# Performance work log

Measured on AMD Instinct MI355X. Metric: run time of the kernel, lower is better.

The kernel has to match this reference:

```python
import jax, jax.numpy as jnp
import numpy as np

N = 50000   # nodes
E = 600000  # directed edges
B = 128     # graphs
IN = 128
H = 128
K = 30      # sort-pool k
C_OUT = 32
KER = 5
OUT_DIM = 10
L_OUT = K - KER + 1  # 26


def setup_inputs() -> dict:
    key = jax.random.key(0)
    ks = jax.random.split(key, 12)
    s = 0.05
    return {
        "x": jax.random.normal(ks[0], (N, IN), jnp.float32),
        "edge_index": jax.random.randint(ks[1], (2, E), 0, N),
        "batch": jnp.sort(jax.random.randint(ks[2], (N,), 0, B)),
        "W0": jax.random.normal(ks[3], (IN, H), jnp.float32) * s,
        "b0": jnp.zeros((H,), jnp.float32),
        "W1": jax.random.normal(ks[4], (H, H), jnp.float32) * s,
        "b1": jnp.zeros((H,), jnp.float32),
        "W2": jax.random.normal(ks[5], (H, H), jnp.float32) * s,
        "b2": jnp.zeros((H,), jnp.float32),
        "conv_w": jax.random.normal(ks[6], (C_OUT, H, KER), jnp.float32) * s,
        "conv_b": jnp.zeros((C_OUT,), jnp.float32),
        "lin1_w": jax.random.normal(ks[7], (C_OUT * L_OUT, H), jnp.float32) * s,
        "lin1_b": jnp.zeros((H,), jnp.float32),
        "lin2_w": jax.random.normal(ks[8], (H, OUT_DIM), jnp.float32) * s,
        "lin2_b": jnp.zeros((OUT_DIM,), jnp.float32),
    }


def reference(x, edge_index, batch, W0, b0, W1, b1, W2, b2,
              conv_w, conv_b, lin1_w, lin1_b, lin2_w, lin2_b):
    # --- GCN normalization (A + I, symmetric deg^-1/2) ---
    loops = jnp.arange(N)
    row = jnp.concatenate([edge_index[0], loops])  # source
    col = jnp.concatenate([edge_index[1], loops])  # target (aggregation side)
    deg = jax.ops.segment_sum(jnp.ones_like(col, dtype=x.dtype), col, num_segments=N)
    dinv = jax.lax.rsqrt(jnp.maximum(deg, 1.0))
    norm = dinv[row] * dinv[col]  # [E+N]

    def gcn(h, W, b):
        hw = h @ W                                            # [N,H]
        msg = hw[row] * norm[:, None]                         # gather [E+N,H]
        return jax.ops.segment_sum(msg, col, num_segments=N) + b

    h = jax.nn.relu(gcn(x, W0, b0))
    h = jax.nn.relu(gcn(h, W1, b1))
    h = jax.nn.relu(gcn(h, W2, b2))

    # --- SortAggregation: per-graph sort by last channel (desc), top-K, zero-pad ---
    last = h[:, -1]
    order = jnp.lexsort((-last, batch))  # primary: batch, secondary: last desc
    hs = h[order]
    bs = batch[order]
    counts = jax.ops.segment_sum(jnp.ones((N,), jnp.int32), batch, num_segments=B)
    starts = jnp.cumsum(counts) - counts  # exclusive prefix sum
    rank = jnp.arange(N) - starts[bs]     # within-graph rank after sort
    r = jnp.where(rank < K, rank, K)      # overflow bucket K is discarded
    pooled = jnp.zeros((B, K + 1, H), h.dtype).at[bs, r].add(hs)[:, :K]  # [B,K,H]

    # --- conv1d head (NCH layout, matches torch view/transpose) ---
    xc = jnp.transpose(pooled, (0, 2, 1))  # [B,H,K]
    y = jax.lax.conv_general_dilated(xc, conv_w, (1,), "VALID",
                                     dimension_numbers=("NCH", "OIH", "NCH"))
    y = jax.nn.relu(y + conv_b[None, :, None])  # [B,C_OUT,L_OUT]
    y = y.reshape(B, -1)
    y = jax.nn.relu(y @ lin1_w + lin1_b)
    return y @ lin2_w + lin2_b  # [B,OUT_DIM]
```

## Files before the change

### kernel.cpp

```cpp
#include <hip/hip_runtime.h>
#include <math.h>

#define Nn 50000
#define Ee 600000
#define Bg 128
#define Hd 128
#define Kt 30
#define CO 32
#define KW 5
#define LOUT 26
#define CAP 2048
#define SCB 196
#define CVO 8

typedef float v2f __attribute__((ext_vector_type(2)));
typedef short bf16x8 __attribute__((ext_vector_type(8)));
typedef float f32x4 __attribute__((ext_vector_type(4)));

__device__ __forceinline__ unsigned short bfr(float v) {
    unsigned u = __builtin_bit_cast(unsigned, v);
    unsigned r = (u + 0x7FFFu + ((u >> 16) & 1u)) >> 16;
    return (unsigned short)r;
}
__device__ __forceinline__ float bff(unsigned short h) {
    unsigned u = ((unsigned)h) << 16;
    return __builtin_bit_cast(float, u);
}

__global__ void init_kernel(int* __restrict__ deg_i, int* __restrict__ cnt,
                            int* __restrict__ bstart,
                            const float* __restrict__ conv_w, float* __restrict__ wT2) {
    int i = blockIdx.x * 256 + threadIdx.x;
    if (i < Nn) { deg_i[i] = 1; cnt[i] = 0; }
    if (i <= Bg) bstart[i] = Nn;
    if (i < CO * KW * Hd) {
        int ci = i & 127;
        int r = i >> 7;
        int o = r / KW, k = r - o * KW;
        wT2[i] = conv_w[((size_t)o * Hd + ci) * KW + k];
    }
}

__global__ void wprep_kernel(const float* __restrict__ W0, const float* __restrict__ W1,
                             const float* __restrict__ W2,
                             ushort* __restrict__ Bph, ushort* __restrict__ Bpm,
                             ushort* __restrict__ Bpl) {
    int t = blockIdx.x * 256 + threadIdx.x;
    if (t >= 3 * 2048) return;
    int l = t >> 11;
    int r = t & 2047;
    int kc = r >> 9;
    int n = (r >> 6) & 7;
    int lane = r & 63;
    int m = lane & 15, kq = lane >> 4;
    const float* W = (l == 0) ? W0 : (l == 1) ? W1 : W2;
    int col = n * 16 + m;
    size_t off = ((size_t)l * 2048 + (size_t)((kc * 8 + n) * 64 + lane)) * 8;
#pragma unroll
    for (int j = 0; j < 8; ++j) {
        float v = W[(size_t)(kc * 32 + kq * 8 + j) * Hd + col];
        unsigned short h = bfr(v);
        float r1 = v - bff(h);
        unsigned short mid = bfr(r1);
        Bph[off + j] = h;
        Bpm[off + j] = mid;
        Bpl[off + j] = bfr(r1 - bff(mid));
    }
}

__global__ void count_kernel(const int* __restrict__ ei, const int* __restrict__ batch,
                             int* __restrict__ deg_i, int* __restrict__ bstart) {
    int i = blockIdx.x * 256 + threadIdx.x;
    if (i < Ee) atomicAdd(&deg_i[ei[Ee + i]], 1);
    if (i < Nn) {
        int b = batch[i];
        if (i == 0) {
            bstart[b] = 0;
        } else {
            int bp = batch[i - 1];
            if (bp != b) bstart[b] = i;
        }
    }
}

__global__ __launch_bounds__(256) void scanA_kernel(const int* __restrict__ deg_i,
                            float* __restrict__ dinv, int* __restrict__ bsum) {
    __shared__ int s[256];
    int tid = threadIdx.x;
    int i = blockIdx.x * 256 + tid;
    int v = 0;
    if (i < Nn) {
        int d = deg_i[i];
        dinv[i] = 1.0f / sqrtf((float)d);
        v = d - 1;
    }
    s[tid] = v;
    __syncthreads();
    for (int off = 128; off > 0; off >>= 1) {
        if (tid < off) s[tid] += s[tid + off];
        __syncthreads();
    }
    if (tid == 0) bsum[blockIdx.x] = s[0];
}

__global__ __launch_bounds__(256) void scanB_kernel(const int* __restrict__ bsum,
                            int* __restrict__ boff, int* __restrict__ bstart) {
    __shared__ int s[256];
    int tid = threadIdx.x;
    int v = (tid < SCB) ? bsum[tid] : 0;
    s[tid] = v;
    __syncthreads();
    for (int off = 1; off < 256; off <<= 1) {
        int t = (tid >= off) ? s[tid - off] : 0;
        __syncthreads();
        s[tid] += t;
        __syncthreads();
    }
    if (tid < SCB) boff[tid] = s[tid] - v;
    if (tid == 0) {
        for (int b = Bg - 1; b >= 0; --b)
            if (bstart[b] == Nn) bstart[b] = bstart[b + 1];
    }
}

__global__ __launch_bounds__(256) void scanC_kernel(const int* __restrict__ deg_i,
                            const int* __restrict__ boff, int* __restrict__ row_ptr) {
    __shared__ int s[256];
    int tid = threadIdx.x;
    int i = blockIdx.x * 256 + tid;
    int v = (i < Nn) ? deg_i[i] - 1 : 0;
    s[tid] = v;
    __syncthreads();
    for (int off = 1; off < 256; off <<= 1) {
        int t = (tid >= off) ? s[tid - off] : 0;
        __syncthreads();
        s[tid] += t;
        __syncthreads();
    }
    if (i < Nn) row_ptr[i + 1] = s[tid] + boff[blockIdx.x];
    if (i == 0) row_ptr[0] = 0;
}

__global__ void fill_kernel(const int* __restrict__ ei, const int* __restrict__ row_ptr,
                            int* __restrict__ cnt, int* __restrict__ csr_src) {
    int e = blockIdx.x * 256 + threadIdx.x;
    if (e >= Ee) return;
    int c = ei[Ee + e];
    int r = ei[e];
    int p = row_ptr[c] + atomicAdd(&cnt[c], 1);
    csr_src[p] = r;
}

__global__ __launch_bounds__(256) void mmx_kernel(const float* __restrict__ Hin,
                            const ushort* __restrict__ Bph, const ushort* __restrict__ Bpm,
                            const ushort* __restrict__ Bpl,
                            const float* __restrict__ dinv, float* __restrict__ hw) {
    int tid = threadIdx.x;
    int w = tid >> 6, lane = tid & 63;
    int m = lane & 15, kq = lane >> 4;
    int rowA = blockIdx.x * 64 + w * 16 + m;
    bool va = rowA < Nn;
    const float* ap = Hin + (size_t)rowA * Hd;
    f32x4 acc[8];
#pragma unroll
    for (int n = 0; n < 8; ++n) acc[n] = (f32x4)0.f;
#pragma unroll
    for (int kc = 0; kc < 4; ++kc) {
        bf16x8 a0 = (bf16x8)0, a1 = (bf16x8)0, a2 = (bf16x8)0;
        if (va) {
            float av[8];
            *(float4*)&av[0] = *(const float4*)(ap + kc * 32 + kq * 8);
            *(float4*)&av[4] = *(const float4*)(ap + kc * 32 + kq * 8 + 4);
#pragma unroll
            for (int j = 0; j < 8; ++j) {
                unsigned short h = bfr(av[j]);
                float r1 = av[j] - bff(h);
                unsigned short mid = bfr(r1);
                a0[j] = (short)h;
                a1[j] = (short)mid;
                a2[j] = (short)bfr(r1 - bff(mid));
            }
        }
        const ushort* bhp = Bph + (size_t)((kc * 8) * 64 + lane) * 8;
        const ushort* bmp = Bpm + (size_t)((kc * 8) * 64 + lane) * 8;
        const ushort* blp = Bpl + (size_t)((kc * 8) * 64 + lane) * 8;
#pragma unroll
        for (int n = 0; n < 8; ++n) {
            bf16x8 b0 = *(const bf16x8*)(bhp + (size_t)n * 64 * 8);
            bf16x8 b1 = *(const bf16x8*)(bmp + (size_t)n * 64 * 8);
            bf16x8 b2 = *(const bf16x8*)(blp + (size_t)n * 64 * 8);
            acc[n] = __builtin_amdgcn_mfma_f32_16x16x32_bf16(a0, b0, acc[n], 0, 0, 0);
            acc[n] = __builtin_amdgcn_mfma_f32_16x16x32_bf16(a1, b0, acc[n], 0, 0, 0);
            acc[n] = __builtin_amdgcn_mfma_f32_16x16x32_bf16(a0, b1, acc[n], 0, 0, 0);
            acc[n] = __builtin_amdgcn_mfma_f32_16x16x32_bf16(a1, b1, acc[n], 0, 0, 0);
            acc[n] = __builtin_amdgcn_mfma_f32_16x16x32_bf16(a2, b0, acc[n], 0, 0, 0);
            acc[n] = __builtin_amdgcn_mfma_f32_16x16x32_bf16(a0, b2, acc[n], 0, 0, 0);
        }
    }
    int rbase = blockIdx.x * 64 + w * 16 + kq * 4;
#pragma unroll
    for (int reg = 0; reg < 4; ++reg) {
        int r = rbase + reg;
        if (r < Nn) {
            float s = dinv[r];
#pragma unroll
            for (int n = 0; n < 8; ++n)
                hw[(size_t)r * Hd + n * 16 + m] = acc[n][reg] * s;
        }
    }
}

__global__ __launch_bounds__(256) void agg_kernel(const float* __restrict__ hw,
                            const int* __restrict__ row_ptr, const int* __restrict__ csr_src,
                            const float* __restrict__ dinv, const float* __restrict__ bias,
                            float* __restrict__ hout) {
    int node = blockIdx.x * 4 + (threadIdx.x >> 6);
    if (node >= Nn) return;
    int lane = threadIdx.x & 63;
    const v2f* hw2 = (const v2f*)hw;
    v2f a0 = hw2[(size_t)node * 64 + lane];
    v2f a1 = 0.f, a2 = 0.f, a3 = 0.f;
    int e0 = row_ptr[node], e1 = row_ptr[node + 1];
    int e = e0;
    for (; e + 3 < e1; e += 4) {
        int s0 = __builtin_nontemporal_load(csr_src + e);
        int s1 = __builtin_nontemporal_load(csr_src + e + 1);
        int s2 = __builtin_nontemporal_load(csr_src + e + 2);
        int s3 = __builtin_nontemporal_load(csr_src + e + 3);
        a0 += hw2[(size_t)s0 * 64 + lane];
        a1 += hw2[(size_t)s1 * 64 + lane];
        a2 += hw2[(size_t)s2 * 64 + lane];
        a3 += hw2[(size_t)s3 * 64 + lane];
    }
    for (; e < e1; ++e) {
        int s0 = __builtin_nontemporal_load(csr_src + e);
        a0 += hw2[(size_t)s0 * 64 + lane];
    }
    v2f acc = (a0 + a1) + (a2 + a3);
    float d = dinv[node];
    v2f bv = ((const v2f*)bias)[lane];
    v2f o;
    o.x = fmaxf(fmaf(d, acc.x, bv.x), 0.f);
    o.y = fmaxf(fmaf(d, acc.y, bv.y), 0.f);
    ((v2f*)hout)[(size_t)node * 64 + lane] = o;
}

__global__ __launch_bounds__(256) void topk_kernel(const float* __restrict__ h,
                            const int* __restrict__ bstart, float* __restrict__ xcg) {
    __shared__ float vals[CAP];
    __shared__ float rv[4];
    __shared__ int ri[4];
    __shared__ int selS[Kt];
    int b = blockIdx.x, tid = threadIdx.x;
    int s0 = bstart[b], s1 = bstart[b + 1];
    int n = s1 - s0;
    int nc = n < CAP ? n : CAP;
    for (int j = tid; j < nc; j += 256)
        vals[j] = h[(size_t)(s0 + j) * Hd + (Hd - 1)];
    __syncthreads();
    for (int k = 0; k < Kt; ++k) {
        float bv = -1.f;
        int bi = 0x7fffffff;
        for (int j = tid; j < nc; j += 256) {
            float v = vals[j];
            if (v > bv || (v == bv && j < bi)) { bv = v; bi = j; }
        }
        for (int off = 32; off > 0; off >>= 1) {
            float ov = __shfl_down(bv, off);
            int oi = __shfl_down(bi, off);
            if (ov > bv || (ov == bv && oi < bi)) { bv = ov; bi = oi; }
        }
        int wid = tid >> 6;
        if ((tid & 63) == 0) { rv[wid] = bv; ri[wid] = bi; }
        __syncthreads();
        if (tid == 0) {
            float fv = rv[0]; int fi = ri[0];
            for (int w = 1; w < 4; ++w) {
                if (rv[w] > fv || (rv[w] == fv && ri[w] < fi)) { fv = rv[w]; fi = ri[w]; }
            }
            if (k < n) {
                selS[k] = s0 + fi;
                vals[fi] = -1.f;
            } else {
                selS[k] = -1;
            }
        }
        __syncthreads();
    }
    for (int i = tid; i < Kt * Hd; i += 256) {
        int t = i >> 7, c = i & 127;
        int s = selS[t];
        xcg[((size_t)b * Kt + t) * Hd + c] = (s >= 0) ? h[(size_t)s * Hd + c] : 0.f;
    }
}

__global__ __launch_bounds__(256) void conv_kernel(const float* __restrict__ xcg,
                            const float* __restrict__ wT2, const float* __restrict__ conv_b,
                            float* __restrict__ flatg) {
    __shared__ float xcl[Kt][130];
    int b = blockIdx.x, q = blockIdx.y;
    int o0 = q * CVO;
    int tid = threadIdx.x;
    for (int i = tid; i < Kt * 32; i += 256) {
        int t = i >> 5, c4 = i & 31;
        float4 v = ((const float4*)(xcg + ((size_t)b * Kt + t) * Hd))[c4];
        float2* dst = (float2*)&xcl[t][c4 * 4];
        dst[0] = make_float2(v.x, v.y);
        dst[1] = make_float2(v.z, v.w);
    }
    __syncthreads();
    int idx = tid;
    if (idx < CVO * LOUT) {
        int op = idx / LOUT, t = idx - op * LOUT;
        int o = o0 + op;
        float acc = conv_b[o];
#pragma unroll
        for (int k = 0; k < KW; ++k) {
            const float* xr = &xcl[t + k][0];
            const float* wr = wT2 + ((size_t)o * KW + k) * Hd;
#pragma unroll 8
            for (int c4 = 0; c4 < 32; ++c4) {
                float2 xa = *(const float2*)(xr + c4 * 4);
                float2 xb = *(const float2*)(xr + c4 * 4 + 2);
                float4 wv = *(const float4*)(wr + c4 * 4);
                acc = fmaf(xa.x, wv.x, acc);
                acc = fmaf(xa.y, wv.y, acc);
                acc = fmaf(xb.x, wv.z, acc);
                acc = fmaf(xb.y, wv.w, acc);
            }
        }
        flatg[((size_t)b * CO + o) * LOUT + t] = fmaxf(acc, 0.f);
    }
}

__global__ __launch_bounds__(256) void head2_kernel(const float* __restrict__ flatg,
                            const float* __restrict__ l1w, const float* __restrict__ l1b,
                            const float* __restrict__ l2w, const float* __restrict__ l2b,
                            float* __restrict__ out) {
    __shared__ float fl[CO * LOUT];
    __shared__ float pz[2][Hd];
    __shared__ float z[Hd];
    int b = blockIdx.x, tid = threadIdx.x;
    for (int i = tid; i < CO * LOUT; i += 256)
        fl[i] = flatg[(size_t)b * (CO * LOUT) + i];
    __syncthreads();
    int hh = tid & 127, half = tid >> 7;
    int m0 = half * 416;
    float acc = 0.f;
#pragma unroll 8
    for (int m = 0; m < 416; ++m)
        acc = fmaf(fl[m0 + m], l1w[(size_t)(m0 + m) * Hd + hh], acc);
    pz[half][hh] = acc;
    __syncthreads();
    if (tid < Hd)
        z[tid] = fmaxf(pz[0][tid] + pz[1][tid] + l1b[tid], 0.f);
    __syncthreads();
    if (tid < 10) {
        float a2 = l2b[tid];
        for (int j = 0; j < Hd; ++j)
            a2 = fmaf(z[j], l2w[j * 10 + tid], a2);
        out[b * 10 + tid] = a2;
    }
}

extern "C" void kernel_launch(void* const* d_in, const int* in_sizes, int n_in,
                              void* d_out, int out_size, void* d_ws, size_t ws_size,
                              hipStream_t stream) {
    const float* x      = (const float*)d_in[0];
    const int*   ei     = (const int*)d_in[1];
    const int*   batch  = (const int*)d_in[2];
    const float* W0     = (const float*)d_in[3];
    const float* b0     = (const float*)d_in[4];
    const float* W1     = (const float*)d_in[5];
    const float* b1     = (const float*)d_in[6];
    const float* W2     = (const float*)d_in[7];
    const float* b2     = (const float*)d_in[8];
    const float* conv_w = (const float*)d_in[9];
    const float* conv_b = (const float*)d_in[10];
    const float* l1w    = (const float*)d_in[11];
    const float* l1b    = (const float*)d_in[12];
    const float* l2w    = (const float*)d_in[13];
    const float* l2b    = (const float*)d_in[14];
    float* out = (float*)d_out;

    int* wsI = (int*)d_ws;
    size_t off = 0;
    int*   deg_i   = wsI + off; off += Nn;
    int*   cnt     = wsI + off; off += Nn;
    int*   row_ptr = wsI + off; off += 50004;
    int*   bstart  = wsI + off; off += 132;
    float* dinv    = (float*)(wsI + off); off += Nn;
    int*   bsum    = wsI + off; off += 256;
    int*   boff    = wsI + off; off += 256;
    int*   csr_src = wsI + off; off += Ee;
    off = (off + 3) & ~(size_t)3;
    ushort* Bph  = (ushort*)(wsI + off); off += 3 * 16384 / 2;
    ushort* Bpm  = (ushort*)(wsI + off); off += 3 * 16384 / 2;
    ushort* Bpl  = (ushort*)(wsI + off); off += 3 * 16384 / 2;
    float* hw    = (float*)(wsI + off); off += (size_t)Nn * Hd;
    float* hbuf  = (float*)(wsI + off); off += (size_t)Nn * Hd;
    float* xcg   = (float*)(wsI + off); off += (size_t)Bg * Kt * Hd;
    float* wT2   = (float*)(wsI + off); off += CO * KW * Hd;
    float* flatg = (float*)(wsI + off); off += (size_t)Bg * CO * LOUT;

    init_kernel<<<(Nn + 255) / 256, 256, 0, stream>>>(deg_i, cnt, bstart, conv_w, wT2);
    wprep_kernel<<<24, 256, 0, stream>>>(W0, W1, W2, Bph, Bpm, Bpl);
    count_kernel<<<(Ee + 255) / 256, 256, 0, stream>>>(ei, batch, deg_i, bstart);
    scanA_kernel<<<SCB, 256, 0, stream>>>(deg_i, dinv, bsum);
    scanB_kernel<<<1, 256, 0, stream>>>(bsum, boff, bstart);
    scanC_kernel<<<SCB, 256, 0, stream>>>(deg_i, boff, row_ptr);
    fill_kernel<<<(Ee + 255) / 256, 256, 0, stream>>>(ei, row_ptr, cnt, csr_src);

    dim3 mmGrid((Nn + 63) / 64);
    dim3 aggGrid((Nn + 3) / 4);
    mmx_kernel<<<mmGrid, 256, 0, stream>>>(x, Bph, Bpm, Bpl, dinv, hw);
    agg_kernel<<<aggGrid, 256, 0, stream>>>(hw, row_ptr, csr_src, dinv, b0, hbuf);
    mmx_kernel<<<mmGrid, 256, 0, stream>>>(hbuf, Bph + 16384, Bpm + 16384, Bpl + 16384, dinv, hw);
    agg_kernel<<<aggGrid, 256, 0, stream>>>(hw, row_ptr, csr_src, dinv, b1, hbuf);
    mmx_kernel<<<mmGrid, 256, 0, stream>>>(hbuf, Bph + 32768, Bpm + 32768, Bpl + 32768, dinv, hw);
    agg_kernel<<<aggGrid, 256, 0, stream>>>(hw, row_ptr, csr_src, dinv, b2, hbuf);

    topk_kernel<<<Bg, 256, 0, stream>>>(hbuf, bstart, xcg);
    conv_kernel<<<dim3(Bg, CO / CVO), 256, 0, stream>>>(xcg, wT2, conv_b, flatg);
    head2_kernel<<<Bg, 256, 0, stream>>>(flatg, l1w, l1b, l2w, l2b, out);
}
```

Measured before the change: 483.9 us.

## Fuse CSR build into cooperative kernel and merge tail kernels

Replaces the count/scan/fill sequence of five launches with one cooperative kernel that uses grid-wide syncs. The init and weight-prep kernels are merged into one launch. The top-k, conv and MLP head kernels become a single per-graph kernel that keeps intermediates in shared memory instead of global scratch. This cuts launch overhead and global round-trips, but the cooperative launch needs 1024 blocks resident at once, the conv stage now runs on only 128 blocks, and grid.sync adds its own cost.

```diff
diff --git a/kernel.cpp b/kernel.cpp
--- a/kernel.cpp
+++ b/kernel.cpp
@@ -1,5 +1,8 @@
 #include <hip/hip_runtime.h>
+#include <hip/hip_cooperative_groups.h>
 #include <math.h>
+
+namespace cg = cooperative_groups;
 
 #define Nn 50000
 #define Ee 600000
@@ -10,8 +13,7 @@
 #define KW 5
 #define LOUT 26
 #define CAP 2048
-#define SCB 196
-#define CVO 8
+#define CG_B 1024
 
 typedef float v2f __attribute__((ext_vector_type(2)));
 typedef short bf16x8 __attribute__((ext_vector_type(8)));
@@ -27,9 +29,13 @@
     return __builtin_bit_cast(float, u);
 }
 
-__global__ void init_kernel(int* __restrict__ deg_i, int* __restrict__ cnt,
+__global__ void initwprep_kernel(int* __restrict__ deg_i, int* __restrict__ cnt,
                             int* __restrict__ bstart,
-                            const float* __restrict__ conv_w, float* __restrict__ wT2) {
+                            const float* __restrict__ conv_w, float* __restrict__ wT2,
+                            const float* __restrict__ W0, const float* __restrict__ W1,
+                            const float* __restrict__ W2,
+                            ushort* __restrict__ Bph, ushort* __restrict__ Bpm,
+                            ushort* __restrict__ Bpl) {
     int i = blockIdx.x * 256 + threadIdx.x;
     if (i < Nn) { deg_i[i] = 1; cnt[i] = 0; }
     if (i <= Bg) bstart[i] = Nn;
@@ -39,116 +45,110 @@
         int o = r / KW, k = r - o * KW;
         wT2[i] = conv_w[((size_t)o * Hd + ci) * KW + k];
     }
-}
-
-__global__ void wprep_kernel(const float* __restrict__ W0, const float* __restrict__ W1,
-                             const float* __restrict__ W2,
-                             ushort* __restrict__ Bph, ushort* __restrict__ Bpm,
-                             ushort* __restrict__ Bpl) {
-    int t = blockIdx.x * 256 + threadIdx.x;
-    if (t >= 3 * 2048) return;
-    int l = t >> 11;
-    int r = t & 2047;
-    int kc = r >> 9;
-    int n = (r >> 6) & 7;
-    int lane = r & 63;
-    int m = lane & 15, kq = lane >> 4;
-    const float* W = (l == 0) ? W0 : (l == 1) ? W1 : W2;
-    int col = n * 16 + m;
-    size_t off = ((size_t)l * 2048 + (size_t)((kc * 8 + n) * 64 + lane)) * 8;
-#pragma unroll
-    for (int j = 0; j < 8; ++j) {
-        float v = W[(size_t)(kc * 32 + kq * 8 + j) * Hd + col];
-        unsigned short h = bfr(v);
-        float r1 = v - bff(h);
-        unsigned short mid = bfr(r1);
-        Bph[off + j] = h;
-        Bpm[off + j] = mid;
-        Bpl[off + j] = bfr(r1 - bff(mid));
-    }
-}
-
-__global__ void count_kernel(const int* __restrict__ ei, const int* __restrict__ batch,
-                             int* __restrict__ deg_i, int* __restrict__ bstart) {
-    int i = blockIdx.x * 256 + threadIdx.x;
-    if (i < Ee) atomicAdd(&deg_i[ei[Ee + i]], 1);
-    if (i < Nn) {
+    if (i < 3 * 2048) {
+        int l = i >> 11;
+        int r = i & 2047;
+        int kc = r >> 9;
+        int n = (r >> 6) & 7;
+        int lane = r & 63;
+        int m = lane & 15, kq = lane >> 4;
+        const float* W = (l == 0) ? W0 : (l == 1) ? W1 : W2;
+        int col = n * 16 + m;
+        size_t off = ((size_t)l * 2048 + (size_t)((kc * 8 + n) * 64 + lane)) * 8;
+#pragma unroll
+        for (int j = 0; j < 8; ++j) {
+            float v = W[(size_t)(kc * 32 + kq * 8 + j) * Hd + col];
+            unsigned short h = bfr(v);
+            float r1 = v - bff(h);
+            unsigned short mid = bfr(r1);
+            Bph[off + j] = h;
+            Bpm[off + j] = mid;
+            Bpl[off + j] = bfr(r1 - bff(mid));
+        }
+    }
+}
+
+__global__ __launch_bounds__(256, 4) void csr_coop(
+        const int* __restrict__ ei, const int* __restrict__ batch,
+        int* __restrict__ deg_i, int* __restrict__ bstart,
+        float* __restrict__ dinv, int* __restrict__ bsum, int* __restrict__ boff,
+        int* __restrict__ row_ptr, int* __restrict__ cnt, int* __restrict__ csr_src) {
+    cg::grid_group grid = cg::this_grid();
+    int tid = threadIdx.x;
+    int gtid = blockIdx.x * 256 + tid;
+    const int T = CG_B * 256;
+    __shared__ int ls[256];
+
+    for (int i = gtid; i < Ee; i += T)
+        atomicAdd(&deg_i[ei[Ee + i]], 1);
+    for (int i = gtid; i < Nn; i += T) {
         int b = batch[i];
-        if (i == 0) {
-            bstart[b] = 0;
-        } else {
-            int bp = batch[i - 1];
-            if (bp != b) bstart[b] = i;
-        }
-    }
-}
-
-__global__ __launch_bounds__(256) void scanA_kernel(const int* __restrict__ deg_i,
-                            float* __restrict__ dinv, int* __restrict__ bsum) {
-    __shared__ int s[256];
-    int tid = threadIdx.x;
-    int i = blockIdx.x * 256 + tid;
-    int v = 0;
-    if (i < Nn) {
-        int d = deg_i[i];
-        dinv[i] = 1.0f / sqrtf((float)d);
-        v = d - 1;
-    }
-    s[tid] = v;
-    __syncthreads();
-    for (int off = 128; off > 0; off >>= 1) {
-        if (tid < off) s[tid] += s[tid + off];
+        if (i == 0) bstart[b] = 0;
+        else if (batch[i - 1] != b) bstart[b] = i;
+    }
+    grid.sync();
+
+    {
+        int v = 0;
+        if (gtid < Nn) {
+            int d = deg_i[gtid];
+            dinv[gtid] = 1.0f / sqrtf((float)d);
+            v = d - 1;
+        }
+        ls[tid] = v;
         __syncthreads();
-    }
-    if (tid == 0) bsum[blockIdx.x] = s[0];
-}
-
-__global__ __launch_bounds__(256) void scanB_kernel(const int* __restrict__ bsum,
-                            int* __restrict__ boff, int* __restrict__ bstart) {
-    __shared__ int s[256];
-    int tid = threadIdx.x;
-    int v = (tid < SCB) ? bsum[tid] : 0;
-    s[tid] = v;
-    __syncthreads();
-    for (int off = 1; off < 256; off <<= 1) {
-        int t = (tid >= off) ? s[tid - off] : 0;
+        for (int off = 128; off > 0; off >>= 1) {
+            if (tid < off) ls[tid] += ls[tid + off];
+            __syncthreads();
+        }
+        if (tid == 0) bsum[blockIdx.x] = ls[0];
+    }
+    grid.sync();
+
+    if (blockIdx.x == 0) {
+        int base = tid * 4;
+        int s0 = bsum[base], s1 = bsum[base + 1], s2 = bsum[base + 2], s3 = bsum[base + 3];
+        ls[tid] = s0 + s1 + s2 + s3;
         __syncthreads();
-        s[tid] += t;
+        for (int off = 1; off < 256; off <<= 1) {
+            int v = (tid >= off) ? ls[tid - off] : 0;
+            __syncthreads();
+            ls[tid] += v;
+            __syncthreads();
+        }
+        int excl = (tid > 0) ? ls[tid - 1] : 0;
+        boff[base]     = excl;
+        boff[base + 1] = excl + s0;
+        boff[base + 2] = excl + s0 + s1;
+        boff[base + 3] = excl + s0 + s1 + s2;
+        if (tid == 0) {
+            for (int b = Bg - 1; b >= 0; --b)
+                if (bstart[b] == Nn) bstart[b] = bstart[b + 1];
+        }
+    }
+    grid.sync();
+
+    {
+        int v = (gtid < Nn) ? deg_i[gtid] - 1 : 0;
+        ls[tid] = v;
         __syncthreads();
-    }
-    if (tid < SCB) boff[tid] = s[tid] - v;
-    if (tid == 0) {
-        for (int b = Bg - 1; b >= 0; --b)
-            if (bstart[b] == Nn) bstart[b] = bstart[b + 1];
-    }
-}
-
-__global__ __launch_bounds__(256) void scanC_kernel(const int* __restrict__ deg_i,
-                            const int* __restrict__ boff, int* __restrict__ row_ptr) {
-    __shared__ int s[256];
-    int tid = threadIdx.x;
-    int i = blockIdx.x * 256 + tid;
-    int v = (i < Nn) ? deg_i[i] - 1 : 0;
-    s[tid] = v;
-    __syncthreads();
-    for (int off = 1; off < 256; off <<= 1) {
-        int t = (tid >= off) ? s[tid - off] : 0;
-        __syncthreads();
-        s[tid] += t;
-        __syncthreads();
-    }
-    if (i < Nn) row_ptr[i + 1] = s[tid] + boff[blockIdx.x];
-    if (i == 0) row_ptr[0] = 0;
-}
-
-__global__ void fill_kernel(const int* __restrict__ ei, const int* __restrict__ row_ptr,
-                            int* __restrict__ cnt, int* __restrict__ csr_src) {
-    int e = blockIdx.x * 256 + threadIdx.x;
-    if (e >= Ee) return;
-    int c = ei[Ee + e];
-    int r = ei[e];
-    int p = row_ptr[c] + atomicAdd(&cnt[c], 1);
-    csr_src[p] = r;
+        for (int off = 1; off < 256; off <<= 1) {
+            int t2 = (tid >= off) ? ls[tid - off] : 0;
+            __syncthreads();
+            ls[tid] += t2;
+            __syncthreads();
+        }
+        if (gtid < Nn) row_ptr[gtid + 1] = ls[tid] + boff[blockIdx.x];
+        if (gtid == 0) row_ptr[0] = 0;
+    }
+    grid.sync();
+
+    for (int e = gtid; e < Ee; e += T) {
+        int c = ei[Ee + e];
+        int r = ei[e];
+        int p = row_ptr[c] + atomicAdd(&cnt[c], 1);
+        csr_src[p] = r;
+    }
 }
 
 __global__ __launch_bounds__(256) void mmx_kernel(const float* __restrict__ Hin,
@@ -245,13 +245,22 @@
     ((v2f*)hout)[(size_t)node * 64 + lane] = o;
 }
 
-__global__ __launch_bounds__(256) void topk_kernel(const float* __restrict__ h,
-                            const int* __restrict__ bstart, float* __restrict__ xcg) {
+__global__ __launch_bounds__(256) void tail_kernel(const float* __restrict__ h,
+                            const int* __restrict__ bstart,
+                            const float* __restrict__ wT2, const float* __restrict__ conv_b,
+                            const float* __restrict__ l1w, const float* __restrict__ l1b,
+                            const float* __restrict__ l2w, const float* __restrict__ l2b,
+                            float* __restrict__ out) {
     __shared__ float vals[CAP];
+    __shared__ float xcl[Kt][130];
+    __shared__ float fl[CO * LOUT];
+    __shared__ float pz[2][Hd];
+    __shared__ float z[Hd];
     __shared__ float rv[4];
     __shared__ int ri[4];
     __shared__ int selS[Kt];
     int b = blockIdx.x, tid = threadIdx.x;
+
     int s0 = bstart[b], s1 = bstart[b + 1];
     int n = s1 - s0;
     int nc = n < CAP ? n : CAP;
@@ -290,29 +299,11 @@
     for (int i = tid; i < Kt * Hd; i += 256) {
         int t = i >> 7, c = i & 127;
         int s = selS[t];
-        xcg[((size_t)b * Kt + t) * Hd + c] = (s >= 0) ? h[(size_t)s * Hd + c] : 0.f;
-    }
-}
-
-__global__ __launch_bounds__(256) void conv_kernel(const float* __restrict__ xcg,
-                            const float* __restrict__ wT2, const float* __restrict__ conv_b,
-                            float* __restrict__ flatg) {
-    __shared__ float xcl[Kt][130];
-    int b = blockIdx.x, q = blockIdx.y;
-    int o0 = q * CVO;
-    int tid = threadIdx.x;
-    for (int i = tid; i < Kt * 32; i += 256) {
-        int t = i >> 5, c4 = i & 31;
-        float4 v = ((const float4*)(xcg + ((size_t)b * Kt + t) * Hd))[c4];
-        float2* dst = (float2*)&xcl[t][c4 * 4];
-        dst[0] = make_float2(v.x, v.y);
-        dst[1] = make_float2(v.z, v.w);
+        xcl[t][c] = (s >= 0) ? h[(size_t)s * Hd + c] : 0.f;
     }
     __syncthreads();
-    int idx = tid;
-    if (idx < CVO * LOUT) {
-        int op = idx / LOUT, t = idx - op * LOUT;
-        int o = o0 + op;
+    for (int oi = tid; oi < CO * LOUT; oi += 256) {
+        int o = oi / LOUT, t = oi - o * LOUT;
         float acc = conv_b[o];
 #pragma unroll
         for (int k = 0; k < KW; ++k) {
@@ -329,20 +320,8 @@
                 acc = fmaf(xb.y, wv.w, acc);
             }
         }
-        flatg[((size_t)b * CO + o) * LOUT + t] = fmaxf(acc, 0.f);
-    }
-}
-
-__global__ __launch_bounds__(256) void head2_kernel(const float* __restrict__ flatg,
-                            const float* __restrict__ l1w, const float* __restrict__ l1b,
-                            const float* __restrict__ l2w, const float* __restrict__ l2b,
-                            float* __restrict__ out) {
-    __shared__ float fl[CO * LOUT];
-    __shared__ float pz[2][Hd];
-    __shared__ float z[Hd];
-    int b = blockIdx.x, tid = threadIdx.x;
-    for (int i = tid; i < CO * LOUT; i += 256)
-        fl[i] = flatg[(size_t)b * (CO * LOUT) + i];
+        fl[oi] = fmaxf(acc, 0.f);
+    }
     __syncthreads();
     int hh = tid & 127, half = tid >> 7;
     int m0 = half * 416;
@@ -390,8 +369,8 @@
     int*   row_ptr = wsI + off; off += 50004;
     int*   bstart  = wsI + off; off += 132;
     float* dinv    = (float*)(wsI + off); off += Nn;
-    int*   bsum    = wsI + off; off += 256;
-    int*   boff    = wsI + off; off += 256;
+    int*   bsum    = wsI + off; off += CG_B;
+    int*   boff    = wsI + off; off += CG_B;
     int*   csr_src = wsI + off; off += Ee;
     off = (off + 3) & ~(size_t)3;
     ushort* Bph  = (ushort*)(wsI + off); off += 3 * 16384 / 2;
@@ -399,17 +378,16 @@
     ushort* Bpl  = (ushort*)(wsI + off); off += 3 * 16384 / 2;
     float* hw    = (float*)(wsI + off); off += (size_t)Nn * Hd;
     float* hbuf  = (float*)(wsI + off); off += (size_t)Nn * Hd;
-    float* xcg   = (float*)(wsI + off); off += (size_t)Bg * Kt * Hd;
     float* wT2   = (float*)(wsI + off); off += CO * KW * Hd;
-    float* flatg = (float*)(wsI + off); off += (size_t)Bg * CO * LOUT;
-
-    init_kernel<<<(Nn + 255) / 256, 256, 0, stream>>>(deg_i, cnt, bstart, conv_w, wT2);
-    wprep_kernel<<<24, 256, 0, stream>>>(W0, W1, W2, Bph, Bpm, Bpl);
-    count_kernel<<<(Ee + 255) / 256, 256, 0, stream>>>(ei, batch, deg_i, bstart);
-    scanA_kernel<<<SCB, 256, 0, stream>>>(deg_i, dinv, bsum);
-    scanB_kernel<<<1, 256, 0, stream>>>(bsum, boff, bstart);
-    scanC_kernel<<<SCB, 256, 0, stream>>>(deg_i, boff, row_ptr);
-    fill_kernel<<<(Ee + 255) / 256, 256, 0, stream>>>(ei, row_ptr, cnt, csr_src);
+
+    initwprep_kernel<<<(Nn + 255) / 256, 256, 0, stream>>>(deg_i, cnt, bstart,
+        conv_w, wT2, W0, W1, W2, Bph, Bpm, Bpl);
+
+    void* cargs[] = { (void*)&ei, (void*)&batch, (void*)&deg_i, (void*)&bstart,
+                      (void*)&dinv, (void*)&bsum, (void*)&boff, (void*)&row_ptr,
+                      (void*)&cnt, (void*)&csr_src };
+    hipLaunchCooperativeKernel((const void*)csr_coop, dim3(CG_B), dim3(256),
+                               cargs, 0, stream);
 
     dim3 mmGrid((Nn + 63) / 64);
     dim3 aggGrid((Nn + 3) / 4);
@@ -420,7 +398,6 @@
     mmx_kernel<<<mmGrid, 256, 0, stream>>>(hbuf, Bph + 32768, Bpm + 32768, Bpl + 32768, dinv, hw);
     agg_kernel<<<aggGrid, 256, 0, stream>>>(hw, row_ptr, csr_src, dinv, b2, hbuf);
 
-    topk_kernel<<<Bg, 256, 0, stream>>>(hbuf, bstart, xcg);
-    conv_kernel<<<dim3(Bg, CO / CVO), 256, 0, stream>>>(xcg, wT2, conv_b, flatg);
-    head2_kernel<<<Bg, 256, 0, stream>>>(flatg, l1w, l1b, l2w, l2b, out);
-}
+    tail_kernel<<<Bg, 256, 0, stream>>>(hbuf, bstart, wT2, conv_b,
+                                        l1w, l1b, l2w, l2b, out);
+}
```

Result: slower. 906.7 us (+87.4%).
